# Kernel tuning notes

Hardware: AMD Instinct MI355X
Metric: run time of the kernel (lower is better)

The kernel has to match this reference:

```python
import math
import jax, jax.numpy as jnp
import numpy as np

D_MODEL = 1024
N_HEADS = 16
D_K = 64


def setup_inputs() -> dict:
    key = jax.random.key(0)
    ks = jax.random.split(key, 12)
    N, T = 4, 2048
    hd = N_HEADS * D_K
    s_in = 1.0 / math.sqrt(D_MODEL)
    s_hd = 1.0 / math.sqrt(hd)
    return {
        "x_k": jax.random.normal(ks[0], (N, T, D_MODEL), jnp.float32),
        "x_v": jax.random.normal(ks[1], (N, T, D_MODEL), jnp.float32),
        "x_q": jax.random.normal(ks[2], (N, T, D_MODEL), jnp.float32),
        "mask": jnp.ones((N, T), jnp.int32),
        "Wk": jax.random.normal(ks[3], (D_MODEL, hd), jnp.float32) * s_in,
        "bk": jax.random.normal(ks[4], (hd,), jnp.float32) * s_in,
        "Wv": jax.random.normal(ks[5], (D_MODEL, hd), jnp.float32) * s_in,
        "bv": jax.random.normal(ks[6], (hd,), jnp.float32) * s_in,
        "Wq": jax.random.normal(ks[7], (D_MODEL, hd), jnp.float32) * s_in,
        "bq": jax.random.normal(ks[8], (hd,), jnp.float32) * s_in,
        "Wf": jax.random.normal(ks[9], (hd, D_MODEL), jnp.float32) * s_hd,
        "bf": jax.random.normal(ks[10], (D_MODEL,), jnp.float32) * s_hd,
    }


def _split_heads(x):  # [N,T,H*D] -> [N,H,T,D]
    n, t, _ = x.shape
    return x.reshape(n, t, N_HEADS, D_K).transpose(0, 2, 1, 3)


def reference(x_k, x_v, x_q, mask, Wk, bk, Wv, bv, Wq, bq, Wf, bf):
    k = _split_heads(x_k @ Wk + bk)  # projected but (faithfully) unused in scores
    v = _split_heads(x_v @ Wv + bv)
    q = _split_heads(x_q @ Wq + bq)
    # NOTE: original code computes scores from q and v (not k) — reproduced faithfully.
    scores = jnp.einsum('nhid,nhjd->nhij', q, v) / math.sqrt(D_K)
    scores = jnp.where(mask[:, None, None, :] == 0, -jnp.inf, scores)
    weights = jax.nn.softmax(scores, axis=-1)
    A = jnp.einsum('nhij,nhjd->nhid', weights, v)  # [N,H,T,D]
    n, h, t, d = A.shape
    A = A.transpose(0, 2, 1, 3).reshape(n, t, h * d)
    return A @ Wf + bf
```

## Files before the change

### kernel.cpp

```cpp
#include <hip/hip_runtime.h>
#include <cstdint>
#include <type_traits>

typedef unsigned short u16;
typedef __attribute__((ext_vector_type(8))) short short8;
typedef __attribute__((ext_vector_type(8))) __fp16 half8;
typedef __attribute__((ext_vector_type(2))) __fp16 half2v;
typedef __attribute__((ext_vector_type(4))) float f32x4;

#define DMODEL 1024
#define TSEQ   2048
#define NHEADS 16
#define DKH    64
#define NBATCH 4
#define MROWS  (NBATCH * TSEQ)
#define QSCALE 0.18033688011f

__device__ __forceinline__ float b2f(u16 u) {
  union { unsigned int u; float f; } c; c.u = ((unsigned int)u) << 16; return c.f;
}
__device__ __forceinline__ u16 f2b(float f) {
  union { float f; unsigned int u; } c; c.f = f;
  unsigned int u = c.u;
  return (u16)((u + 0x7fffu + ((u >> 16) & 1u)) >> 16);
}
__device__ __forceinline__ half2v pkrtz(float a, float b) {
  return __builtin_amdgcn_cvt_pkrtz(a, b);
}
__device__ __forceinline__ unsigned h2u(half2v h) {
  unsigned u; __builtin_memcpy(&u, &h, 4); return u;
}
__device__ __forceinline__ u16 f2h(float f) {
  half2v h = pkrtz(f, 0.f);
  u16 u; __builtin_memcpy(&u, &h, 2); return u;
}

__device__ __forceinline__ void gl_lds16(const u16* g, u16* l) {
  __builtin_amdgcn_global_load_lds((const __attribute__((address_space(1))) void*)g,
                                   (__attribute__((address_space(3))) void*)l, 16, 0, 0);
}

__global__ void cvt_bf16(const float* __restrict__ in, u16* __restrict__ out) {
  int i = blockIdx.x * 256 + threadIdx.x;
  const float4* p = (const float4*)in + (long long)i * 2;
  float4 a = p[0], b = p[1];
  union { u16 s[8]; uint4 v; } pk;
  pk.s[0] = f2b(a.x); pk.s[1] = f2b(a.y); pk.s[2] = f2b(a.z); pk.s[3] = f2b(a.w);
  pk.s[4] = f2b(b.x); pk.s[5] = f2b(b.y); pk.s[6] = f2b(b.z); pk.s[7] = f2b(b.w);
  ((uint4*)out)[i] = pk.v;
}

template <bool F16>
__global__ void transpose_cvt(const float* __restrict__ in, u16* __restrict__ out) {
  __shared__ float t[32][33];
  int bx = blockIdx.x * 32, by = blockIdx.y * 32;
  int tx = threadIdx.x, ty = threadIdx.y;
  #pragma unroll
  for (int i = ty; i < 32; i += 8)
    t[i][tx] = in[(by + i) * DMODEL + bx + tx];
  __syncthreads();
  #pragma unroll
  for (int i = ty; i < 32; i += 8)
    out[(bx + i) * DMODEL + by + tx] = F16 ? f2h(t[tx][i]) : f2b(t[tx][i]);
}

__global__ void transpose_v(const u16* __restrict__ Vb, u16* __restrict__ VbT) {
  __shared__ u16 tl[64 * 66];
  int tb = blockIdx.x, h = blockIdx.y, nb = blockIdx.z;
  int tx = threadIdx.x, ty = threadIdx.y;
  long long src = (long long)(nb * TSEQ + tb * 64) * DMODEL + h * DKH;
  #pragma unroll
  for (int r = ty; r < 64; r += 4)
    tl[r * 66 + tx] = Vb[src + (long long)r * DMODEL + tx];
  __syncthreads();
  long long dst = (long long)((nb * NHEADS + h) * DKH) * TSEQ + tb * 64;
  #pragma unroll
  for (int r = ty; r < 64; r += 4)
    VbT[dst + (long long)r * TSEQ + tx] = f2h(b2f(tl[tx * 66 + r]));
}

template <bool F16, typename CT>
__device__ __forceinline__ void gemm_core(
    u16* As, u16* Bs,
    const u16* __restrict__ A, const u16* __restrict__ Bt,
    const float* __restrict__ bias, CT* __restrict__ C,
    const int bm, const int bn, const float osc) {
  const int tid  = threadIdx.x;
  const int wv   = tid >> 6, lane = tid & 63;
  const int wm   = wv >> 1, wn = wv & 1;
  const int l15  = lane & 15, quad = lane >> 4;
  const int srow = lane >> 3, gch = (lane & 7) ^ srow;

  f32x4 acc[4][4];
  #pragma unroll
  for (int i = 0; i < 4; ++i)
    #pragma unroll
    for (int j = 0; j < 4; ++j)
      acc[i][j] = (f32x4){0.f, 0.f, 0.f, 0.f};

  const u16* Ag = A  + (long long)(bm * 128) * DMODEL;
  const u16* Bg = Bt + (long long)(bn * 128) * DMODEL;

  for (int k0 = 0; k0 < DMODEL; k0 += 64) {
    __syncthreads();
    #pragma unroll
    for (int j = 0; j < 4; ++j) {
      int rb = wv * 32 + j * 8;
      gl_lds16(Ag + (long long)(rb + srow) * DMODEL + k0 + gch * 8, As + rb * 64);
      gl_lds16(Bg + (long long)(rb + srow) * DMODEL + k0 + gch * 8, Bs + rb * 64);
    }
    __syncthreads();
    #pragma unroll
    for (int ks = 0; ks < 2; ++ks) {
      #pragma unroll
      for (int mi = 0; mi < 4; ++mi) {
        int ra = wm * 64 + mi * 16 + l15;
        const u16* pa = As + ra * 64 + (((ks * 4 + quad) ^ (ra & 7)) * 8);
        #pragma unroll
        for (int ni = 0; ni < 4; ++ni) {
          int rb = wn * 64 + ni * 16 + l15;
          const u16* pb = Bs + rb * 64 + (((ks * 4 + quad) ^ (rb & 7)) * 8);
          if constexpr (F16)
            acc[mi][ni] = __builtin_amdgcn_mfma_f32_16x16x32_f16(
                *(const half8*)pa, *(const half8*)pb, acc[mi][ni], 0, 0, 0);
          else
            acc[mi][ni] = __builtin_amdgcn_mfma_f32_16x16x32_bf16(
                *(const short8*)pa, *(const short8*)pb, acc[mi][ni], 0, 0, 0);
        }
      }
    }
  }

  #pragma unroll
  for (int ni = 0; ni < 4; ++ni) {
    int col = bn * 128 + wn * 64 + ni * 16 + l15;
    float bvf = bias[col];
    #pragma unroll
    for (int mi = 0; mi < 4; ++mi) {
      int row0 = bm * 128 + wm * 64 + mi * 16 + quad * 4;
      #pragma unroll
      for (int r = 0; r < 4; ++r) {
        float val = (acc[mi][ni][r] + bvf) * osc;
        long long idx = (long long)(row0 + r) * DMODEL + col;
        if constexpr (std::is_same_v<CT, float>) C[idx] = val;
        else                                     C[idx] = f2b(val);
      }
    }
  }
}

__global__ __launch_bounds__(256, 4)
void gemm_qv(const u16* __restrict__ Xq, const u16* __restrict__ Xv,
             const u16* __restrict__ WqT, const u16* __restrict__ WvT,
             const float* __restrict__ bq, const float* __restrict__ bv,
             u16* __restrict__ Qb, u16* __restrict__ Vb) {
  __shared__ u16 As[128 * 64];
  __shared__ u16 Bs[128 * 64];
  const bool isq = (blockIdx.z == 0);
  gemm_core<false, u16>(As, Bs, isq ? Xq : Xv, isq ? WqT : WvT,
                        isq ? bq : bv, isq ? Qb : Vb,
                        blockIdx.x, blockIdx.y, isq ? QSCALE : 1.0f);
}

__global__ __launch_bounds__(256, 2)
void gemm_out(const u16* __restrict__ A, const u16* __restrict__ Bt,
              const float* __restrict__ bias, float* __restrict__ C) {
  __shared__ u16 As[128 * 64];
  __shared__ u16 Bs[128 * 64];
  gemm_core<true, float>(As, Bs, A, Bt, bias, C, blockIdx.x, blockIdx.y, 1.0f);
}

__global__ __launch_bounds__(256, 4)
void attn_kernel(const u16* __restrict__ Qb, const u16* __restrict__ Vb,
                 const u16* __restrict__ VbTh, const int* __restrict__ mask,
                 u16* __restrict__ Ab) {
  __shared__ u16 Vs[64 * 64];
  __shared__ u16 Vts[64 * 64];
  __shared__ u16 Ps[4 * 32 * 72];
  __shared__ float Msf[64];

  const int tid  = threadIdx.x;
  const int qblk = blockIdx.x, h = blockIdx.y, nb = blockIdx.z;
  const int wv   = tid >> 6, lane = tid & 63;
  const int l15  = lane & 15, quad = lane >> 4;
  const int srow = lane >> 3, gch = (lane & 7) ^ srow;

  const int q0 = qblk * 128 + wv * 32;
  const long long rowbase = (long long)nb * TSEQ;
  const long long hd = (long long)((nb * NHEADS + h) * DKH);
  u16* psb = Ps + wv * 32 * 72;

  short8 qf[2][2];
  #pragma unroll
  for (int mi = 0; mi < 2; ++mi)
    #pragma unroll
    for (int ks = 0; ks < 2; ++ks)
      qf[mi][ks] = *(const short8*)(Qb + (rowbase + q0 + mi * 16 + l15) * DMODEL
                                    + h * DKH + ks * 32 + quad * 8);

  f32x4 of[2][4];
  #pragma unroll
  for (int mi = 0; mi < 2; ++mi)
    #pragma unroll
    for (int dt = 0; dt < 4; ++dt)
      of[mi][dt] = (f32x4){0.f, 0.f, 0.f, 0.f};
  float lsum[2] = {0.f, 0.f};
  const half2v one2 = {(__fp16)1.f, (__fp16)1.f};

  for (int vb = 0; vb < TSEQ / 64; ++vb) {
    __syncthreads();
    #pragma unroll
    for (int j = 0; j < 2; ++j) {
      int rb = wv * 16 + j * 8;
      gl_lds16(Vb   + (rowbase + vb * 64 + rb + srow) * DMODEL + h * DKH + gch * 8, Vs  + rb * 64);
      gl_lds16(VbTh + (hd + rb + srow) * TSEQ + vb * 64 + gch * 8,                  Vts + rb * 64);
    }
    int mv = mask[nb * TSEQ + vb * 64 + lane];
    if (tid < 64) Msf[tid] = mv ? 0.f : -INFINITY;
    const bool slowm = __any(mv == 0);
    __syncthreads();

    f32x4 st[2][4];
    #pragma unroll
    for (int mi = 0; mi < 2; ++mi)
      #pragma unroll
      for (int tt = 0; tt < 4; ++tt)
        st[mi][tt] = (f32x4){0.f, 0.f, 0.f, 0.f};
    #pragma unroll
    for (int tt = 0; tt < 4; ++tt) {
      int r = tt * 16 + l15;
      #pragma unroll
      for (int ks = 0; ks < 2; ++ks) {
        short8 vf = *(const short8*)(Vs + r * 64 + (((ks * 4 + quad) ^ (l15 & 7)) * 8));
        #pragma unroll
        for (int mi = 0; mi < 2; ++mi)
          st[mi][tt] = __builtin_amdgcn_mfma_f32_16x16x32_bf16(vf, qf[mi][ks], st[mi][tt], 0, 0, 0);
      }
    }

    f32x4 msk[4];
    if (slowm) {
      #pragma unroll
      for (int tt = 0; tt < 4; ++tt)
        msk[tt] = *(const f32x4*)(Msf + tt * 16 + quad * 4);
    }
    #pragma unroll
    for (int mi = 0; mi < 2; ++mi) {
      #pragma unroll
      for (int tt = 0; tt < 4; ++tt) {
        float a0 = st[mi][tt][0], a1 = st[mi][tt][1];
        float a2 = st[mi][tt][2], a3 = st[mi][tt][3];
        if (slowm) { a0 += msk[tt][0]; a1 += msk[tt][1]; a2 += msk[tt][2]; a3 += msk[tt][3]; }
        float p0 = __builtin_amdgcn_exp2f(a0);
        float p1 = __builtin_amdgcn_exp2f(a1);
        float p2 = __builtin_amdgcn_exp2f(a2);
        float p3 = __builtin_amdgcn_exp2f(a3);
        half2v h01 = pkrtz(p0, p1), h23 = pkrtz(p2, p3);
#if __has_builtin(__builtin_amdgcn_fdot2)
        lsum[mi] = __builtin_amdgcn_fdot2(h01, one2, lsum[mi], false);
        lsum[mi] = __builtin_amdgcn_fdot2(h23, one2, lsum[mi], false);
#else
        lsum[mi] += (p0 + p1) + (p2 + p3);
#endif
        uint2 pk; pk.x = h2u(h01); pk.y = h2u(h23);
        *(uint2*)(psb + (mi * 16 + l15) * 72 + tt * 16 + quad * 4) = pk;
      }
    }

    #pragma unroll
    for (int kc = 0; kc < 2; ++kc) {
      half8 pf[2];
      #pragma unroll
      for (int mi = 0; mi < 2; ++mi)
        pf[mi] = *(const half8*)(psb + (mi * 16 + l15) * 72 + kc * 32 + quad * 8);
      #pragma unroll
      for (int dt = 0; dt < 4; ++dt) {
        int r = dt * 16 + l15;
        half8 vtf = *(const half8*)(Vts + r * 64 + (((kc * 4 + quad) ^ (l15 & 7)) * 8));
        #pragma unroll
        for (int mi = 0; mi < 2; ++mi)
          of[mi][dt] = __builtin_amdgcn_mfma_f32_16x16x32_f16(vtf, pf[mi], of[mi][dt], 0, 0, 0);
      }
    }
  }

  #pragma unroll
  for (int mi = 0; mi < 2; ++mi) {
    float l = lsum[mi];
    l += __shfl_xor(l, 16, 64);
    l += __shfl_xor(l, 32, 64);
    float inv = 1.0f / l;
    long long row = rowbase + q0 + mi * 16 + l15;
    #pragma unroll
    for (int dt = 0; dt < 4; ++dt) {
      uint2 o;
      o.x = h2u(pkrtz(of[mi][dt][0] * inv, of[mi][dt][1] * inv));
      o.y = h2u(pkrtz(of[mi][dt][2] * inv, of[mi][dt][3] * inv));
      *(uint2*)(Ab + row * DMODEL + h * DKH + dt * 16 + quad * 4) = o;
    }
  }
}

extern "C" void kernel_launch(void* const* d_in, const int* in_sizes, int n_in,
                              void* d_out, int out_size, void* d_ws, size_t ws_size,
                              hipStream_t stream) {
  const float* x_v  = (const float*)d_in[1];
  const float* x_q  = (const float*)d_in[2];
  const int*   mask = (const int*)d_in[3];
  const float* Wv   = (const float*)d_in[6];
  const float* bv   = (const float*)d_in[7];
  const float* Wq   = (const float*)d_in[8];
  const float* bq   = (const float*)d_in[9];
  const float* Wf   = (const float*)d_in[10];
  const float* bfp  = (const float*)d_in[11];

  char* w = (char*)d_ws;
  u16* WqT  = (u16*)(w + 0);
  u16* WvT  = (u16*)(w + (2ll << 20));
  u16* WfT  = (u16*)(w + (4ll << 20));
  u16* Xq   = (u16*)(w + (6ll << 20));
  u16* Xv   = (u16*)(w + (22ll << 20));
  u16* Qb   = (u16*)(w + (38ll << 20));
  u16* Vb   = (u16*)(w + (54ll << 20));
  u16* VbTh = (u16*)(w + (70ll << 20));
  u16* Ab   = Xq;

  dim3 tb(32, 8), tg(32, 32);
  transpose_cvt<false><<<tg, tb, 0, stream>>>(Wq, WqT);
  transpose_cvt<false><<<tg, tb, 0, stream>>>(Wv, WvT);
  transpose_cvt<true ><<<tg, tb, 0, stream>>>(Wf, WfT);

  cvt_bf16<<<MROWS * DMODEL / 8 / 256, 256, 0, stream>>>(x_q, Xq);
  cvt_bf16<<<MROWS * DMODEL / 8 / 256, 256, 0, stream>>>(x_v, Xv);

  gemm_qv<<<dim3(MROWS / 128, DMODEL / 128, 2), 256, 0, stream>>>(
      Xq, Xv, WqT, WvT, bq, bv, Qb, Vb);

  transpose_v<<<dim3(TSEQ / 64, NHEADS, NBATCH), dim3(64, 4), 0, stream>>>(Vb, VbTh);

  attn_kernel<<<dim3(TSEQ / 128, NHEADS, NBATCH), 256, 0, stream>>>(Qb, Vb, VbTh, mask, Ab);

  gemm_out<<<dim3(MROWS / 128, DMODEL / 128), 256, 0, stream>>>(Ab, WfT, bfp, (float*)d_out);
}
```

Baseline: 323.4 us.

## Shrink GEMM N-tile, merge small launches, compute softmax rowsum via MFMA

The GEMM tile is cut from 128x128 to 128x64, A/B fragments are hoisted into registers, and launch bounds are raised to target more resident blocks per CU. The three weight-transpose launches and the two activation-convert launches are each merged into one launch indexed by blockIdx.z, saving launch overhead. In attention, the per-lane fdot2 row-sum plus cross-lane shuffles is replaced by an extra MFMA against a ones vector that accumulates the softmax denominator. The smaller tile lowers per-block data reuse, so more global/LDS traffic is spent per FLOP in exchange for occupancy.

```diff
diff --git a/kernel.cpp b/kernel.cpp
--- a/kernel.cpp
+++ b/kernel.cpp
@@ -40,7 +40,10 @@
                                    (__attribute__((address_space(3))) void*)l, 16, 0, 0);
 }
 
-__global__ void cvt_bf16(const float* __restrict__ in, u16* __restrict__ out) {
+__global__ void cvt_bf16(const float* __restrict__ in0, u16* __restrict__ out0,
+                         const float* __restrict__ in1, u16* __restrict__ out1) {
+  const float* in = blockIdx.z ? in1 : in0;
+  u16* out = blockIdx.z ? out1 : out0;
   int i = blockIdx.x * 256 + threadIdx.x;
   const float4* p = (const float4*)in + (long long)i * 2;
   float4 a = p[0], b = p[1];
@@ -50,8 +53,12 @@
   ((uint4*)out)[i] = pk.v;
 }
 
-template <bool F16>
-__global__ void transpose_cvt(const float* __restrict__ in, u16* __restrict__ out) {
+__global__ void transpose_cvt(const float* __restrict__ w0, u16* __restrict__ o0,
+                              const float* __restrict__ w1, u16* __restrict__ o1,
+                              const float* __restrict__ w2, u16* __restrict__ o2) {
+  const int z = blockIdx.z;
+  const float* in = (z == 0) ? w0 : (z == 1) ? w1 : w2;
+  u16* out = (z == 0) ? o0 : (z == 1) ? o1 : o2;
   __shared__ float t[32][33];
   int bx = blockIdx.x * 32, by = blockIdx.y * 32;
   int tx = threadIdx.x, ty = threadIdx.y;
@@ -61,7 +68,7 @@
   __syncthreads();
   #pragma unroll
   for (int i = ty; i < 32; i += 8)
-    out[(bx + i) * DMODEL + by + tx] = F16 ? f2h(t[tx][i]) : f2b(t[tx][i]);
+    out[(bx + i) * DMODEL + by + tx] = (z == 2) ? f2h(t[tx][i]) : f2b(t[tx][i]);
 }
 
 __global__ void transpose_v(const u16* __restrict__ Vb, u16* __restrict__ VbT) {
@@ -91,15 +98,15 @@
   const int l15  = lane & 15, quad = lane >> 4;
   const int srow = lane >> 3, gch = (lane & 7) ^ srow;
 
-  f32x4 acc[4][4];
+  f32x4 acc[4][2];
   #pragma unroll
   for (int i = 0; i < 4; ++i)
     #pragma unroll
-    for (int j = 0; j < 4; ++j)
+    for (int j = 0; j < 2; ++j)
       acc[i][j] = (f32x4){0.f, 0.f, 0.f, 0.f};
 
   const u16* Ag = A  + (long long)(bm * 128) * DMODEL;
-  const u16* Bg = Bt + (long long)(bn * 128) * DMODEL;
+  const u16* Bg = Bt + (long long)(bn * 64) * DMODEL;
 
   for (int k0 = 0; k0 < DMODEL; k0 += 64) {
     __syncthreads();
@@ -107,33 +114,43 @@
     for (int j = 0; j < 4; ++j) {
       int rb = wv * 32 + j * 8;
       gl_lds16(Ag + (long long)(rb + srow) * DMODEL + k0 + gch * 8, As + rb * 64);
+    }
+    #pragma unroll
+    for (int j = 0; j < 2; ++j) {
+      int rb = wv * 16 + j * 8;
       gl_lds16(Bg + (long long)(rb + srow) * DMODEL + k0 + gch * 8, Bs + rb * 64);
     }
     __syncthreads();
     #pragma unroll
     for (int ks = 0; ks < 2; ++ks) {
+      short8 af[4], bf_[2];
       #pragma unroll
       for (int mi = 0; mi < 4; ++mi) {
         int ra = wm * 64 + mi * 16 + l15;
-        const u16* pa = As + ra * 64 + (((ks * 4 + quad) ^ (ra & 7)) * 8);
+        af[mi] = *(const short8*)(As + ra * 64 + (((ks * 4 + quad) ^ (ra & 7)) * 8));
+      }
+      #pragma unroll
+      for (int ni = 0; ni < 2; ++ni) {
+        int rb = wn * 32 + ni * 16 + l15;
+        bf_[ni] = *(const short8*)(Bs + rb * 64 + (((ks * 4 + quad) ^ (rb & 7)) * 8));
+      }
+      #pragma unroll
+      for (int mi = 0; mi < 4; ++mi)
         #pragma unroll
-        for (int ni = 0; ni < 4; ++ni) {
-          int rb = wn * 64 + ni * 16 + l15;
-          const u16* pb = Bs + rb * 64 + (((ks * 4 + quad) ^ (rb & 7)) * 8);
+        for (int ni = 0; ni < 2; ++ni) {
           if constexpr (F16)
             acc[mi][ni] = __builtin_amdgcn_mfma_f32_16x16x32_f16(
-                *(const half8*)pa, *(const half8*)pb, acc[mi][ni], 0, 0, 0);
+                *(const half8*)&af[mi], *(const half8*)&bf_[ni], acc[mi][ni], 0, 0, 0);
           else
             acc[mi][ni] = __builtin_amdgcn_mfma_f32_16x16x32_bf16(
-                *(const short8*)pa, *(const short8*)pb, acc[mi][ni], 0, 0, 0);
+                af[mi], bf_[ni], acc[mi][ni], 0, 0, 0);
         }
-      }
-    }
-  }
-
-  #pragma unroll
-  for (int ni = 0; ni < 4; ++ni) {
-    int col = bn * 128 + wn * 64 + ni * 16 + l15;
+    }
+  }
+
+  #pragma unroll
+  for (int ni = 0; ni < 2; ++ni) {
+    int col = bn * 64 + wn * 32 + ni * 16 + l15;
     float bvf = bias[col];
     #pragma unroll
     for (int mi = 0; mi < 4; ++mi) {
@@ -149,24 +166,24 @@
   }
 }
 
-__global__ __launch_bounds__(256, 4)
+__global__ __launch_bounds__(256, 6)
 void gemm_qv(const u16* __restrict__ Xq, const u16* __restrict__ Xv,
              const u16* __restrict__ WqT, const u16* __restrict__ WvT,
              const float* __restrict__ bq, const float* __restrict__ bv,
              u16* __restrict__ Qb, u16* __restrict__ Vb) {
   __shared__ u16 As[128 * 64];
-  __shared__ u16 Bs[128 * 64];
+  __shared__ u16 Bs[64 * 64];
   const bool isq = (blockIdx.z == 0);
   gemm_core<false, u16>(As, Bs, isq ? Xq : Xv, isq ? WqT : WvT,
                         isq ? bq : bv, isq ? Qb : Vb,
                         blockIdx.x, blockIdx.y, isq ? QSCALE : 1.0f);
 }
 
-__global__ __launch_bounds__(256, 2)
+__global__ __launch_bounds__(256, 6)
 void gemm_out(const u16* __restrict__ A, const u16* __restrict__ Bt,
               const float* __restrict__ bias, float* __restrict__ C) {
   __shared__ u16 As[128 * 64];
-  __shared__ u16 Bs[128 * 64];
+  __shared__ u16 Bs[64 * 64];
   gemm_core<true, float>(As, Bs, A, Bt, bias, C, blockIdx.x, blockIdx.y, 1.0f);
 }
 
@@ -199,13 +216,16 @@
                                     + h * DKH + ks * 32 + quad * 8);
 
   f32x4 of[2][4];
-  #pragma unroll
-  for (int mi = 0; mi < 2; ++mi)
+  f32x4 lacc[2];
+  #pragma unroll
+  for (int mi = 0; mi < 2; ++mi) {
+    lacc[mi] = (f32x4){0.f, 0.f, 0.f, 0.f};
     #pragma unroll
     for (int dt = 0; dt < 4; ++dt)
       of[mi][dt] = (f32x4){0.f, 0.f, 0.f, 0.f};
-  float lsum[2] = {0.f, 0.f};
-  const half2v one2 = {(__fp16)1.f, (__fp16)1.f};
+  }
+  const half8 ones8 = {(__fp16)1.f, (__fp16)1.f, (__fp16)1.f, (__fp16)1.f,
+                       (__fp16)1.f, (__fp16)1.f, (__fp16)1.f, (__fp16)1.f};
 
   for (int vb = 0; vb < TSEQ / 64; ++vb) {
     __syncthreads();
@@ -255,14 +275,7 @@
         float p1 = __builtin_amdgcn_exp2f(a1);
         float p2 = __builtin_amdgcn_exp2f(a2);
         float p3 = __builtin_amdgcn_exp2f(a3);
-        half2v h01 = pkrtz(p0, p1), h23 = pkrtz(p2, p3);
-#if __has_builtin(__builtin_amdgcn_fdot2)
-        lsum[mi] = __builtin_amdgcn_fdot2(h01, one2, lsum[mi], false);
-        lsum[mi] = __builtin_amdgcn_fdot2(h23, one2, lsum[mi], false);
-#else
-        lsum[mi] += (p0 + p1) + (p2 + p3);
-#endif
-        uint2 pk; pk.x = h2u(h01); pk.y = h2u(h23);
+        uint2 pk; pk.x = h2u(pkrtz(p0, p1)); pk.y = h2u(pkrtz(p2, p3));
         *(uint2*)(psb + (mi * 16 + l15) * 72 + tt * 16 + quad * 4) = pk;
       }
     }
@@ -273,6 +286,9 @@
       #pragma unroll
       for (int mi = 0; mi < 2; ++mi)
         pf[mi] = *(const half8*)(psb + (mi * 16 + l15) * 72 + kc * 32 + quad * 8);
+      #pragma unroll
+      for (int mi = 0; mi < 2; ++mi)
+        lacc[mi] = __builtin_amdgcn_mfma_f32_16x16x32_f16(ones8, pf[mi], lacc[mi], 0, 0, 0);
       #pragma unroll
       for (int dt = 0; dt < 4; ++dt) {
         int r = dt * 16 + l15;
@@ -286,10 +302,7 @@
 
   #pragma unroll
   for (int mi = 0; mi < 2; ++mi) {
-    float l = lsum[mi];
-    l += __shfl_xor(l, 16, 64);
-    l += __shfl_xor(l, 32, 64);
-    float inv = 1.0f / l;
+    float inv = 1.0f / lacc[mi][0];
     long long row = rowbase + q0 + mi * 16 + l15;
     #pragma unroll
     for (int dt = 0; dt < 4; ++dt) {
@@ -325,20 +338,16 @@
   u16* VbTh = (u16*)(w + (70ll << 20));
   u16* Ab   = Xq;
 
-  dim3 tb(32, 8), tg(32, 32);
-  transpose_cvt<false><<<tg, tb, 0, stream>>>(Wq, WqT);
-  transpose_cvt<false><<<tg, tb, 0, stream>>>(Wv, WvT);
-  transpose_cvt<true ><<<tg, tb, 0, stream>>>(Wf, WfT);
-
-  cvt_bf16<<<MROWS * DMODEL / 8 / 256, 256, 0, stream>>>(x_q, Xq);
-  cvt_bf16<<<MROWS * DMODEL / 8 / 256, 256, 0, stream>>>(x_v, Xv);
-
-  gemm_qv<<<dim3(MROWS / 128, DMODEL / 128, 2), 256, 0, stream>>>(
+  transpose_cvt<<<dim3(32, 32, 3), dim3(32, 8), 0, stream>>>(Wq, WqT, Wv, WvT, Wf, WfT);
+
+  cvt_bf16<<<dim3(MROWS * DMODEL / 8 / 256, 1, 2), 256, 0, stream>>>(x_q, Xq, x_v, Xv);
+
+  gemm_qv<<<dim3(MROWS / 128, DMODEL / 64, 2), 256, 0, stream>>>(
       Xq, Xv, WqT, WvT, bq, bv, Qb, Vb);
 
   transpose_v<<<dim3(TSEQ / 64, NHEADS, NBATCH), dim3(64, 4), 0, stream>>>(Vb, VbTh);
 
   attn_kernel<<<dim3(TSEQ / 128, NHEADS, NBATCH), 256, 0, stream>>>(Qb, Vb, VbTh, mask, Ab);
 
-  gemm_out<<<dim3(MROWS / 128, DMODEL / 128), 256, 0, stream>>>(Ab, WfT, bfp, (float*)d_out);
-}
+  gemm_out<<<dim3(MROWS / 128, DMODEL / 64), 256, 0, stream>>>(Ab, WfT, bfp, (float*)d_out);
+}
```

After: 367.4 us. 1.14x slower.
